# Kernel optimization log

Hardware: AMD Instinct MI355X
Metric: run time of the kernel (lower is better)

The kernel has to match this reference:

```python
import jax, jax.numpy as jnp
import numpy as np

NEG_SLOPE = 0.2  # PyG GATConv default negative_slope
EPS = 1e-16


def gat_conv(x, W, att_src, att_dst, bias, src, dst, heads, out_ch, concat):
    """PyG-style GATConv (eval mode, self-loops already included in src/dst).
    x: [N, F_in]; W: [heads*out_ch, F_in]; att_src/att_dst: [1, heads, out_ch]; bias: [heads*out_ch] or [out_ch].
    """
    N = x.shape[0]
    h = (x @ W.T).reshape(N, heads, out_ch)            # [N, H, C]
    a_src = (h * att_src).sum(-1)                      # [N, H]
    a_dst = (h * att_dst).sum(-1)                      # [N, H]
    alpha = jax.nn.leaky_relu(a_src[src] + a_dst[dst], NEG_SLOPE)  # [E, H]
    # segment softmax over destination nodes
    amax = jax.ops.segment_max(alpha, dst, num_segments=N)         # [N, H]
    ex = jnp.exp(alpha - amax[dst])
    denom = jax.ops.segment_sum(ex, dst, num_segments=N)           # [N, H]
    coef = ex / (denom[dst] + EPS)                                 # [E, H]
    out = jax.ops.segment_sum(h[src] * coef[:, :, None], dst, num_segments=N)  # [N, H, C]
    if concat:
        out = out.reshape(N, heads * out_ch)
    else:
        out = out.mean(axis=1)
    return out + bias


def setup_inputs() -> dict:
    key = jax.random.key(0)
    ks = jax.random.split(key, 10)
    N, F_in, H, C, OUT, E = 50000, 128, 4, 64, 2, 800000
    x = jax.random.normal(ks[0], (N, F_in), dtype=jnp.float32)
    edge_index = jax.random.randint(ks[1], (2, E), 0, N, dtype=jnp.int64)
    glorot = lambda k, shp: jax.random.normal(k, shp, dtype=jnp.float32) * jnp.sqrt(2.0 / (shp[0] + shp[-1]))
    W1 = glorot(ks[2], (H * C, F_in))
    att_src1 = glorot(ks[3], (1, H, C))
    att_dst1 = glorot(ks[4], (1, H, C))
    b1 = jnp.zeros((H * C,), dtype=jnp.float32)
    W2 = glorot(ks[5], (1 * OUT, H * C))
    att_src2 = glorot(ks[6], (1, 1, OUT))
    att_dst2 = glorot(ks[7], (1, 1, OUT))
    b2 = jnp.zeros((OUT,), dtype=jnp.float32)
    return {"x": x, "edge_index": edge_index, "W1": W1, "att_src1": att_src1,
            "att_dst1": att_dst1, "b1": b1, "W2": W2, "att_src2": att_src2,
            "att_dst2": att_dst2, "b2": b2}


def reference(x, edge_index, W1, att_src1, att_dst1, b1, W2, att_src2, att_dst2, b2):
    N = x.shape[0]
    loop = jnp.arange(N, dtype=edge_index.dtype)
    src = jnp.concatenate([edge_index[0], loop])   # add self-loops (PyG default)
    dst = jnp.concatenate([edge_index[1], loop])
    h = gat_conv(x, W1, att_src1, att_dst1, b1, src, dst, heads=4, out_ch=64, concat=True)
    h = jax.nn.relu(h)
    out = gat_conv(h, W2, att_src2, att_dst2, b2, src, dst, heads=1, out_ch=2, concat=False)
    return out
```

## Files before the change

### kernel.cpp

```cpp
#include <hip/hip_runtime.h>
#include <hip/hip_bf16.h>
#include <stdint.h>

#define NEG_SLOPE 0.2f
#define EPSV 1e-16f
#define SLOT 64

typedef __attribute__((ext_vector_type(8))) short bf16x8;
typedef __attribute__((ext_vector_type(4))) float f32x4;

static __device__ __forceinline__ float b2f(unsigned short u) {
    union { float f; uint32_t i; } v; v.i = ((uint32_t)u) << 16; return v.f;
}
static __device__ __forceinline__ uint32_t qpk(float a, float b) {
    union { float f; uint32_t u; } x, y; x.f = a; y.f = b;
    return ((x.u + 0x8000u) >> 16) | ((y.u + 0x8000u) & 0xFFFF0000u);
}

static __device__ __forceinline__ void edge_sd(const int* __restrict__ ei,
                                               int e, int E, int& s, int& d) {
    if (e < E) { s = ei[e]; d = ei[E + e]; }
    else       { s = e - E; d = s; }
}

static __device__ __forceinline__ float edge_exp(float as, float ad) {
    float a = as + ad;
    a = a > 0.f ? a : NEG_SLOPE * a;
    return __expf(a);
}

__global__ __launch_bounds__(256) void fused_front_kernel(
    const float* __restrict__ x, const float* __restrict__ W1,
    const float* __restrict__ att_src1, const float* __restrict__ att_dst1,
    const float* __restrict__ b1, const float* __restrict__ W2,
    const int* __restrict__ ei, int E, int ET,
    unsigned short* __restrict__ h1,
    float4* __restrict__ a_src1v, float4* __restrict__ a_dst1v,
    int* __restrict__ deg, unsigned short* __restrict__ csr16,
    float* __restrict__ b1p, float* __restrict__ w2p0, float* __restrict__ w2p1,
    int N, int nblk_gemm, int nblk_edge)
{
    const int b = blockIdx.x, t = threadIdx.x;

    if (b < nblk_gemm) {
        const int wv = t >> 6, lane = t & 63;
        const int l15 = lane & 15, quad = lane >> 4;
        const int m0 = b * 128 + wv * 32;

        union { bf16x8 v; uint32_t u[4]; } A[2][4];
        #pragma unroll
        for (int ms = 0; ms < 2; ++ms) {
            int m = m0 + ms * 16 + l15;
            int mr = m < N ? m : N - 1;
            const float* ap = x + (size_t)mr * 128 + quad * 8;
            #pragma unroll
            for (int kk = 0; kk < 4; ++kk) {
                float4 u0 = *(const float4*)(ap + kk * 32);
                float4 u1 = *(const float4*)(ap + kk * 32 + 4);
                A[ms][kk].u[0] = qpk(u0.x, u0.y);
                A[ms][kk].u[1] = qpk(u0.z, u0.w);
                A[ms][kk].u[2] = qpk(u1.x, u1.y);
                A[ms][kk].u[3] = qpk(u1.z, u1.w);
            }
        }

        f32x4 acc[2][16];
        #pragma unroll
        for (int ms = 0; ms < 2; ++ms)
            #pragma unroll
            for (int ct = 0; ct < 16; ++ct)
                acc[ms][ct] = (f32x4){0.f, 0.f, 0.f, 0.f};

        #pragma unroll
        for (int kk = 0; kk < 4; ++kk) {
            const float* bpr = W1 + (size_t)l15 * 128 + kk * 32 + quad * 8;
            bf16x8 B[16];
            #pragma unroll
            for (int ct = 0; ct < 16; ++ct) {
                const float* bp = bpr + (size_t)ct * 16 * 128;
                float4 u0 = *(const float4*)(bp);
                float4 u1 = *(const float4*)(bp + 4);
                union { bf16x8 v; uint32_t u[4]; } Bv;
                Bv.u[0] = qpk(u0.x, u0.y);
                Bv.u[1] = qpk(u0.z, u0.w);
                Bv.u[2] = qpk(u1.x, u1.y);
                Bv.u[3] = qpk(u1.z, u1.w);
                B[ct] = Bv.v;
            }
            #pragma unroll
            for (int ct = 0; ct < 16; ++ct) {
                acc[0][ct] = __builtin_amdgcn_mfma_f32_16x16x32_bf16(A[0][kk].v, B[ct], acc[0][ct], 0, 0, 0);
                acc[1][ct] = __builtin_amdgcn_mfma_f32_16x16x32_bf16(A[1][kk].v, B[ct], acc[1][ct], 0, 0, 0);
            }
        }

        #pragma unroll
        for (int ms = 0; ms < 2; ++ms) {
            #pragma unroll
            for (int r = 0; r < 4; ++r) {
                int m = m0 + ms * 16 + quad * 4 + r;
                if (m < N) {
                    uint32_t u[8];
                    #pragma unroll
                    for (int j = 0; j < 8; ++j)
                        u[j] = qpk(acc[ms][2 * j][r], acc[ms][2 * j + 1][r]);
                    uint4* hp = (uint4*)(h1 + (size_t)m * 256 + l15 * 16);
                    hp[0] = make_uint4(u[0], u[1], u[2], u[3]);
                    hp[1] = make_uint4(u[4], u[5], u[6], u[7]);
                }
            }
        }

        float as_l[16], ad_l[16];
        #pragma unroll
        for (int ct = 0; ct < 16; ++ct) {
            as_l[ct] = att_src1[ct * 16 + l15];
            ad_l[ct] = att_dst1[ct * 16 + l15];
        }
        #pragma unroll
        for (int ms = 0; ms < 2; ++ms) {
            #pragma unroll
            for (int r = 0; r < 4; ++r) {
                float ps[4] = {0.f, 0.f, 0.f, 0.f};
                float pd[4] = {0.f, 0.f, 0.f, 0.f};
                #pragma unroll
                for (int ct = 0; ct < 16; ++ct) {
                    ps[ct >> 2] += acc[ms][ct][r] * as_l[ct];
                    pd[ct >> 2] += acc[ms][ct][r] * ad_l[ct];
                }
                #pragma unroll
                for (int off = 1; off < 16; off <<= 1) {
                    #pragma unroll
                    for (int hh = 0; hh < 4; ++hh) {
                        ps[hh] += __shfl_xor(ps[hh], off);
                        pd[hh] += __shfl_xor(pd[hh], off);
                    }
                }
                int m = m0 + ms * 16 + quad * 4 + r;
                if (l15 == 0 && m < N) {
                    a_src1v[m] = make_float4(ps[0], ps[1], ps[2], ps[3]);
                    a_dst1v[m] = make_float4(pd[0], pd[1], pd[2], pd[3]);
                }
            }
        }
    } else if (b < nblk_gemm + nblk_edge) {
        int e0 = (b - nblk_gemm) * 512 + t;
        if (e0 < ET) {
            int s, d; edge_sd(ei, e0, E, s, d);
            int rank = atomicAdd(&deg[d], 1);
            csr16[(size_t)d * SLOT + rank] = (unsigned short)s;
        }
        int e1 = e0 + 256;
        if (e1 < ET) {
            int s, d; edge_sd(ei, e1, E, s, d);
            int rank = atomicAdd(&deg[d], 1);
            csr16[(size_t)d * SLOT + rank] = (unsigned short)s;
        }
    } else {
        int cp = t;
        int c = (cp & 15) * 16 + (cp >> 4);
        b1p[cp]  = b1[c];
        w2p0[cp] = W2[c];
        w2p1[cp] = W2[256 + c];
    }
}

__global__ __launch_bounds__(256) void agg1_layer2_kernel(
    const int* __restrict__ deg, const unsigned short* __restrict__ csr16,
    const float* __restrict__ a_src1, const float* __restrict__ a_dst1,
    const unsigned short* __restrict__ h1,
    const float* __restrict__ b1p,
    const float* __restrict__ w2p0, const float* __restrict__ w2p1,
    const float* __restrict__ as2, const float* __restrict__ ad2,
    float4* __restrict__ h2pk, int N)
{
    const int wv = threadIdx.x >> 6, lane = threadIdx.x & 63;
    const int half = lane >> 5, ll = lane & 31;
    const int n = blockIdx.x * 4 + wv;
    if (n >= N) return;
    const int h0 = (ll & 1) * 2;
    const unsigned short* cs = csr16 + (size_t)n * SLOT;
    const int dn = deg[n];
    const float2 adh = *(const float2*)(a_dst1 + (size_t)n * 4 + h0);

    float acc[8] = {0.f, 0.f, 0.f, 0.f, 0.f, 0.f, 0.f, 0.f};
    float den0 = 0.f, den1 = 0.f;

    int i = half;
    int s0 = (i < dn) ? (int)cs[i] : -1;
    int s1 = (i + 2 < dn) ? (int)cs[i + 2] : -1;
    float2 as0 = make_float2(0.f, 0.f);
    uint4 r0 = make_uint4(0, 0, 0, 0);
    if (s0 >= 0) {
        as0 = *(const float2*)(a_src1 + (size_t)s0 * 4 + h0);
        r0 = *(const uint4*)(h1 + (size_t)s0 * 256 + ll * 8);
    }
    while (s0 >= 0) {
        int s2 = (i + 4 < dn) ? (int)cs[i + 4] : -1;
        float2 as1 = make_float2(0.f, 0.f);
        uint4 r1 = make_uint4(0, 0, 0, 0);
        if (s1 >= 0) {
            as1 = *(const float2*)(a_src1 + (size_t)s1 * 4 + h0);
            r1 = *(const uint4*)(h1 + (size_t)s1 * 256 + ll * 8);
        }
        float e0 = edge_exp(as0.x, adh.x);
        float e1 = edge_exp(as0.y, adh.y);
        den0 += e0; den1 += e1;
        acc[0] += e0 * b2f((unsigned short)(r0.x & 0xFFFF));
        acc[1] += e0 * b2f((unsigned short)(r0.x >> 16));
        acc[2] += e0 * b2f((unsigned short)(r0.y & 0xFFFF));
        acc[3] += e0 * b2f((unsigned short)(r0.y >> 16));
        acc[4] += e1 * b2f((unsigned short)(r0.z & 0xFFFF));
        acc[5] += e1 * b2f((unsigned short)(r0.z >> 16));
        acc[6] += e1 * b2f((unsigned short)(r0.w & 0xFFFF));
        acc[7] += e1 * b2f((unsigned short)(r0.w >> 16));
        s0 = s1; as0 = as1; r0 = r1; s1 = s2; i += 2;
    }

    #pragma unroll
    for (int k = 0; k < 8; ++k) acc[k] += __shfl_xor(acc[k], 32);
    den0 += __shfl_xor(den0, 32);
    den1 += __shfl_xor(den1, 32);

    const float inv0 = 1.f / (den0 + EPSV);
    const float inv1 = 1.f / (den1 + EPSV);
    const int c0 = ll * 8;
    float4 ba = *(const float4*)(b1p + c0);
    float4 bb = *(const float4*)(b1p + c0 + 4);
    float v[8];
    v[0] = acc[0] * inv0 + ba.x; v[1] = acc[1] * inv0 + ba.y;
    v[2] = acc[2] * inv0 + ba.z; v[3] = acc[3] * inv0 + ba.w;
    v[4] = acc[4] * inv1 + bb.x; v[5] = acc[5] * inv1 + bb.y;
    v[6] = acc[6] * inv1 + bb.z; v[7] = acc[7] * inv1 + bb.w;
    #pragma unroll
    for (int k = 0; k < 8; ++k) v[k] = v[k] > 0.f ? v[k] : 0.f;

    float4 w0a = *(const float4*)(w2p0 + c0);
    float4 w0b = *(const float4*)(w2p0 + c0 + 4);
    float4 w1a = *(const float4*)(w2p1 + c0);
    float4 w1b = *(const float4*)(w2p1 + c0 + 4);
    float p0 = v[0]*w0a.x + v[1]*w0a.y + v[2]*w0a.z + v[3]*w0a.w
             + v[4]*w0b.x + v[5]*w0b.y + v[6]*w0b.z + v[7]*w0b.w;
    float p1 = v[0]*w1a.x + v[1]*w1a.y + v[2]*w1a.z + v[3]*w1a.w
             + v[4]*w1b.x + v[5]*w1b.y + v[6]*w1b.z + v[7]*w1b.w;
    #pragma unroll
    for (int off = 16; off; off >>= 1) {
        p0 += __shfl_xor(p0, off);
        p1 += __shfl_xor(p1, off);
    }
    if (lane == 0) {
        h2pk[n] = make_float4(p0, p1,
                              p0 * as2[0] + p1 * as2[1],
                              p0 * ad2[0] + p1 * ad2[1]);
    }
}

__global__ __launch_bounds__(256) void aggregate2_csr_kernel(
    const int* __restrict__ deg, const unsigned short* __restrict__ csr16,
    const float4* __restrict__ h2pk,
    const float* __restrict__ b2, float* __restrict__ out, int N)
{
    const int wv = threadIdx.x >> 6, lane = threadIdx.x & 63;
    const int g = lane >> 4, q = lane & 15;
    const int n = blockIdx.x * 16 + wv * 4 + g;
    if (n >= N) return;
    const unsigned short* cs = csr16 + (size_t)n * SLOT;
    const int dn = deg[n];
    float ad = h2pk[n].w;
    float den = 0.f, num0 = 0.f, num1 = 0.f;
    for (int i = q; i < dn; i += 16) {
        int s = (int)cs[i];
        float4 hq = h2pk[s];
        float ex = edge_exp(hq.z, ad);
        den  += ex;
        num0 += ex * hq.x;
        num1 += ex * hq.y;
    }
    #pragma unroll
    for (int off = 8; off; off >>= 1) {
        den  += __shfl_xor(den, off);
        num0 += __shfl_xor(num0, off);
        num1 += __shfl_xor(num1, off);
    }
    if (q == 0) {
        float inv = 1.f / (den + EPSV);
        out[(size_t)n * 2]     = num0 * inv + b2[0];
        out[(size_t)n * 2 + 1] = num1 * inv + b2[1];
    }
}

extern "C" void kernel_launch(void* const* d_in, const int* in_sizes, int n_in,
                              void* d_out, int out_size, void* d_ws, size_t ws_size,
                              hipStream_t stream)
{
    const float* x   = (const float*)d_in[0];
    const int*   ei  = (const int*)d_in[1];
    const float* W1  = (const float*)d_in[2];
    const float* as1 = (const float*)d_in[3];
    const float* ad1 = (const float*)d_in[4];
    const float* b1  = (const float*)d_in[5];
    const float* W2  = (const float*)d_in[6];
    const float* as2 = (const float*)d_in[7];
    const float* ad2 = (const float*)d_in[8];
    const float* b2p = (const float*)d_in[9];

    const int N  = in_sizes[0] / 128;
    const int E  = in_sizes[1] / 2;
    const int ET = E + N;

    char* ws = (char*)d_ws;
    size_t off = 0;
    auto alloc = [&](size_t bytes) -> char* {
        char* p = ws + off;
        off = (off + bytes + 255) & ~(size_t)255;
        return p;
    };
    unsigned short* h1 = (unsigned short*)alloc((size_t)N * 256 * 2);
    float* a_src1  = (float*)alloc((size_t)N * 4 * 4);
    float* a_dst1  = (float*)alloc((size_t)N * 4 * 4);
    float4* h2pk   = (float4*)alloc((size_t)N * 16);
    float* b1pp    = (float*)alloc((size_t)256 * 4);
    float* w2p0    = (float*)alloc((size_t)256 * 4);
    float* w2p1    = (float*)alloc((size_t)256 * 4);
    int*   deg     = (int*)alloc((size_t)N * 4);
    unsigned short* csr16 = (unsigned short*)alloc((size_t)N * SLOT * 2);

    hipMemsetAsync(deg, 0, (size_t)N * 4, stream);

    const int nblk_gemm = (N + 127) / 128;
    const int nblk_edge = (ET + 511) / 512;
    fused_front_kernel<<<nblk_gemm + nblk_edge + 1, 256, 0, stream>>>(
        x, W1, as1, ad1, b1, W2, ei, E, ET,
        h1, (float4*)a_src1, (float4*)a_dst1,
        deg, csr16, b1pp, w2p0, w2p1, N, nblk_gemm, nblk_edge);
    agg1_layer2_kernel<<<(N + 3) / 4, 256, 0, stream>>>(
        deg, csr16, a_src1, a_dst1, h1,
        b1pp, w2p0, w2p1, as2, ad2, h2pk, N);
    aggregate2_csr_kernel<<<(N + 15) / 16, 256, 0, stream>>>(
        deg, csr16, h2pk, b2p, (float*)d_out, N);
}
```

Baseline: 219.5 us.

## Partition CSR build by destination residue to keep scatter atomics XCD-local

The edge-to-CSR scatter phase now gives each group of 8 consecutive blocks a 2048-edge chunk. Each block uses `b & 7` to keep only the edges whose destination satisfies `d % 8 == part`, reading the destination indices with int4 vector loads. Since blocks are dispatched round-robin over the 8 XCDs, each destination's atomics and csr16 row writes should then stay on one XCD's L2, avoiding cross-die coherence traffic. In exchange, every block reads all 2048 destination indices, so destination-index reads are duplicated 8x. The deg array cache lines are still shared across partitions.

Result: slower. 241.7 us (+10.1%).

```diff
diff --git a/kernel.cpp b/kernel.cpp
--- a/kernel.cpp
+++ b/kernel.cpp
@@ -15,12 +15,6 @@
 static __device__ __forceinline__ uint32_t qpk(float a, float b) {
     union { float f; uint32_t u; } x, y; x.f = a; y.f = b;
     return ((x.u + 0x8000u) >> 16) | ((y.u + 0x8000u) & 0xFFFF0000u);
-}
-
-static __device__ __forceinline__ void edge_sd(const int* __restrict__ ei,
-                                               int e, int E, int& s, int& d) {
-    if (e < E) { s = ei[e]; d = ei[E + e]; }
-    else       { s = e - E; d = s; }
 }
 
 static __device__ __forceinline__ float edge_exp(float as, float ad) {
@@ -144,17 +138,35 @@
             }
         }
     } else if (b < nblk_gemm + nblk_edge) {
-        int e0 = (b - nblk_gemm) * 512 + t;
-        if (e0 < ET) {
-            int s, d; edge_sd(ei, e0, E, s, d);
-            int rank = atomicAdd(&deg[d], 1);
-            csr16[(size_t)d * SLOT + rank] = (unsigned short)s;
-        }
-        int e1 = e0 + 256;
-        if (e1 < ET) {
-            int s, d; edge_sd(ei, e1, E, s, d);
-            int rank = atomicAdd(&deg[d], 1);
-            csr16[(size_t)d * SLOT + rank] = (unsigned short)s;
+        const int j = b - nblk_gemm;
+        const int part = b & 7;
+        const int base = (j >> 3) * 2048 + t * 8;
+        if (base + 7 < E) {
+            int4 d0 = *(const int4*)(ei + E + base);
+            int4 d1 = *(const int4*)(ei + E + base + 4);
+            int dv[8] = {d0.x, d0.y, d0.z, d0.w, d1.x, d1.y, d1.z, d1.w};
+            #pragma unroll
+            for (int k = 0; k < 8; ++k) {
+                int d = dv[k];
+                if ((d & 7) == part) {
+                    int s = ei[base + k];
+                    int rank = atomicAdd(&deg[d], 1);
+                    csr16[(size_t)d * SLOT + rank] = (unsigned short)s;
+                }
+            }
+        } else {
+            #pragma unroll
+            for (int k = 0; k < 8; ++k) {
+                int e = base + k;
+                if (e < ET) {
+                    int d = (e < E) ? ei[E + e] : e - E;
+                    if ((d & 7) == part) {
+                        int s = (e < E) ? ei[e] : d;
+                        int rank = atomicAdd(&deg[d], 1);
+                        csr16[(size_t)d * SLOT + rank] = (unsigned short)s;
+                    }
+                }
+            }
         }
     } else {
         int cp = t;
@@ -328,7 +340,7 @@
     hipMemsetAsync(deg, 0, (size_t)N * 4, stream);
 
     const int nblk_gemm = (N + 127) / 128;
-    const int nblk_edge = (ET + 511) / 512;
+    const int nblk_edge = 8 * ((ET + 2047) / 2048);
     fused_front_kernel<<<nblk_gemm + nblk_edge + 1, 256, 0, stream>>>(
         x, W1, as1, ad1, b1, W2, ei, E, ET,
         h1, (float4*)a_src1, (float4*)a_dst1,
```
